# Kernel optimization log

Measured on AMD Instinct MI355X. Metric: run time of the kernel, lower is better.

The kernel has to match this reference:

```python
import jax, jax.numpy as jnp
import numpy as np

N = 50000
E = 800000
DIM_IN = 128
DIM_H = 16
HEADS = 8
DIM_OUT = 16
NEG_SLOPE = 0.2


def setup_inputs() -> dict:
    key = jax.random.key(0)
    ks = jax.random.split(key, 12)
    def glorot(k, shape):
        fan_in = shape[0]
        return jax.random.normal(k, shape, dtype=jnp.float32) / np.sqrt(fan_in)
    x = jax.random.normal(ks[0], (N, DIM_IN), dtype=jnp.float32)
    edge_index = jax.random.randint(ks[1], (2, E), 0, N, dtype=jnp.int64)
    # layer 1: GATv2Conv(dim_in, dim_h, heads=8)
    Wl1 = glorot(ks[2], (DIM_IN, HEADS * DIM_H))
    Wr1 = glorot(ks[3], (DIM_IN, HEADS * DIM_H))
    att1 = glorot(ks[4], (HEADS, DIM_H))
    bias1 = jnp.zeros((HEADS * DIM_H,), dtype=jnp.float32)
    # layer 2: GATv2Conv(dim_h*heads, dim_out, heads=1)
    Wl2 = glorot(ks[5], (HEADS * DIM_H, DIM_OUT))
    Wr2 = glorot(ks[6], (HEADS * DIM_H, DIM_OUT))
    att2 = glorot(ks[7], (1, DIM_OUT))
    bias2 = jnp.zeros((DIM_OUT,), dtype=jnp.float32)
    return {"x": x, "edge_index": edge_index, "Wl1": Wl1, "Wr1": Wr1,
            "att1": att1, "bias1": bias1, "Wl2": Wl2, "Wr2": Wr2,
            "att2": att2, "bias2": bias2}


def gatv2_layer(x, src, dst, Wl, Wr, att, bias, n_nodes, heads, ch):
    # x: [N, F_in]; src/dst: [Etot] (self-loops included)
    xl = (x @ Wl).reshape(n_nodes, heads, ch)  # source transform
    xr = (x @ Wr).reshape(n_nodes, heads, ch)  # target transform
    e = jax.nn.leaky_relu(xl[src] + xr[dst], NEG_SLOPE)      # [Etot, H, C]
    logits = jnp.einsum('ehc,hc->eh', e, att)                # [Etot, H]
    # segment softmax over incoming edges of each target node
    m = jax.ops.segment_max(logits, dst, num_segments=n_nodes)
    a = jnp.exp(logits - m[dst])
    denom = jax.ops.segment_sum(a, dst, num_segments=n_nodes)
    alpha = a / denom[dst]                                   # [Etot, H]
    out = jax.ops.segment_sum(xl[src] * alpha[:, :, None], dst,
                              num_segments=n_nodes)          # [N, H, C]
    return out.reshape(n_nodes, heads * ch) + bias


def reference(x, edge_index, Wl1, Wr1, att1, bias1, Wl2, Wr2, att2, bias2):
    # PyG GATv2Conv adds self-loops by default
    loops = jnp.arange(N, dtype=edge_index.dtype)
    src = jnp.concatenate([edge_index[0], loops])
    dst = jnp.concatenate([edge_index[1], loops])
    # dropout is identity in eval mode
    h = gatv2_layer(x, src, dst, Wl1, Wr1, att1, bias1, N, HEADS, DIM_H)
    h = jax.nn.elu(h)
    h = gatv2_layer(h, src, dst, Wl2, Wr2, att2, bias2, N, 1, DIM_OUT)
    return h, jax.nn.log_softmax(h, axis=1)
```

## Files before the change

kernel.cpp:

```cpp
#include <hip/hip_runtime.h>
#include <hip/hip_bf16.h>
#include <math.h>

#define NN 50000
#define EE 800000
#define DIN 128
#define HEADS 8
#define DH 16
#define DOUT 16
#define NEG 0.2f
#define GM 32
#define GB ((NN + GM - 1) / GM)
#define NB ((NN + 255) / 256)
#define DEGB ((EE / 4 + 255) / 256)
#define PAD 64

typedef __attribute__((ext_vector_type(8))) short bf16x8;
typedef __attribute__((ext_vector_type(4))) float f32x4;

__device__ __forceinline__ unsigned pack2bf(float a, float b) {
    union { __hip_bfloat162 h; unsigned u; } c;
    c.h = __float22bfloat162_rn(make_float2(a, b));
    return c.u;
}
__device__ __forceinline__ unsigned short f2bf(float v) {
    union { __hip_bfloat16 h; unsigned short u; } c;
    c.h = __float2bfloat16(v);
    return c.u;
}
__device__ __forceinline__ float bflo(unsigned u) { return __uint_as_float(u << 16); }
__device__ __forceinline__ float bfhi(unsigned u) { return __uint_as_float(u & 0xffff0000u); }

__global__ __launch_bounds__(256) void init_wcvt(int* __restrict__ cnt,
                                                 int* __restrict__ esrcPad,
                                                 const float* __restrict__ Wl,
                                                 const float* __restrict__ Wr,
                                                 unsigned short* __restrict__ Wb,
                                                 const float* __restrict__ Wl2,
                                                 const float* __restrict__ Wr2,
                                                 unsigned short* __restrict__ Wb2) {
    int b = blockIdx.x, t = threadIdx.x;
    if (b < NB) {
        int i = b * 256 + t;
        if (i < NN) {
            cnt[i] = 1;
            esrcPad[(size_t)i * PAD] = i;
        }
    } else if (b < NB + 128) {
        int i = (b - NB) * 256 + t;
        int n = i >> 7, k = i & 127;
        float v = (n < 128) ? Wl[k * 128 + n] : Wr[k * 128 + (n - 128)];
        Wb[i] = f2bf(v);
    } else {
        int i = (b - NB - 128) * 256 + t;
        int n = i >> 7, k = i & 127;
        float v = (n < 16) ? Wl2[k * 16 + n] : Wr2[k * 16 + (n - 16)];
        Wb2[i] = f2bf(v);
    }
}

__global__ __launch_bounds__(256) void fill_gemm1(const int* __restrict__ ei,
                                                  int* __restrict__ cnt,
                                                  int* __restrict__ esrcPad,
                                                  const float* __restrict__ x,
                                                  const unsigned short* __restrict__ Wb,
                                                  unsigned short* __restrict__ xlb,
                                                  float* __restrict__ xr) {
    __shared__ unsigned short As[GM][136];
    int t = threadIdx.x;
    if (blockIdx.x < DEGB) {
        int i = blockIdx.x * 256 + t;
        if (i >= EE / 4) return;
        int4 ss = ((const int4*)ei)[i];
        int4 dd = ((const int4*)(ei + EE))[i];
        int p;
        p = atomicAdd(&cnt[dd.x], 1); esrcPad[(size_t)dd.x * PAD + p] = ss.x;
        p = atomicAdd(&cnt[dd.y], 1); esrcPad[(size_t)dd.y * PAD + p] = ss.y;
        p = atomicAdd(&cnt[dd.z], 1); esrcPad[(size_t)dd.z * PAD + p] = ss.z;
        p = atomicAdd(&cnt[dd.w], 1); esrcPad[(size_t)dd.w * PAD + p] = ss.w;
        return;
    }
    int n0 = (blockIdx.x - DEGB) * GM;
    {
        int row = t >> 3, seg = t & 7;
        int nsrc = n0 + row < NN ? n0 + row : NN - 1;
        const float4* xp = (const float4*)(x + (size_t)nsrc * DIN + 16 * seg);
        float4 v0 = xp[0], v1 = xp[1], v2 = xp[2], v3 = xp[3];
        uint4 p0 = make_uint4(pack2bf(v0.x, v0.y), pack2bf(v0.z, v0.w),
                              pack2bf(v1.x, v1.y), pack2bf(v1.z, v1.w));
        uint4 p1 = make_uint4(pack2bf(v2.x, v2.y), pack2bf(v2.z, v2.w),
                              pack2bf(v3.x, v3.y), pack2bf(v3.z, v3.w));
        *(uint4*)&As[row][16 * seg]     = p0;
        *(uint4*)&As[row][16 * seg + 8] = p1;
    }
    __syncthreads();
    int lane = t & 63, w = t >> 6;
    int m = lane & 15, quad = lane >> 4;
    f32x4 acc[2][4];
#pragma unroll
    for (int mt = 0; mt < 2; ++mt)
#pragma unroll
        for (int nt = 0; nt < 4; ++nt) acc[mt][nt] = (f32x4){0.f, 0.f, 0.f, 0.f};
#pragma unroll
    for (int ks = 0; ks < 4; ++ks) {
        int k = 32 * ks + 8 * quad;
        bf16x8 a0 = *(const bf16x8*)&As[m][k];
        bf16x8 a1 = *(const bf16x8*)&As[16 + m][k];
#pragma unroll
        for (int nt = 0; nt < 4; ++nt) {
            int n = 64 * w + 16 * nt + m;
            bf16x8 b = *(const bf16x8*)(Wb + (size_t)n * 128 + k);
            acc[0][nt] = __builtin_amdgcn_mfma_f32_16x16x32_bf16(a0, b, acc[0][nt], 0, 0, 0);
            acc[1][nt] = __builtin_amdgcn_mfma_f32_16x16x32_bf16(a1, b, acc[1][nt], 0, 0, 0);
        }
    }
#pragma unroll
    for (int mt = 0; mt < 2; ++mt) {
#pragma unroll
        for (int nt = 0; nt < 4; ++nt) {
            int col = 64 * w + 16 * nt + m;
            int rbase = n0 + 16 * mt + 4 * quad;
            if (col < 128) {
#pragma unroll
                for (int r = 0; r < 4; ++r) {
                    int row = rbase + r;
                    if (row < NN) xlb[(size_t)row * DIN + col] = f2bf(acc[mt][nt][r]);
                }
            } else {
#pragma unroll
                for (int r = 0; r < 4; ++r) {
                    int row = rbase + r;
                    if (row < NN) xr[(size_t)row * DIN + (col - 128)] = acc[mt][nt][r];
                }
            }
        }
    }
}

__global__ __launch_bounds__(256) void l1_fused(const int* __restrict__ esrcPad,
                                                const int* __restrict__ cnt,
                                                const unsigned short* __restrict__ xlb,
                                                const float* __restrict__ xr,
                                                const float* __restrict__ att,
                                                const float* __restrict__ bias,
                                                unsigned short* __restrict__ hb) {
    int d = blockIdx.x * 4 + (threadIdx.x >> 6);
    int lane = threadIdx.x & 63;
    int quarter = lane >> 4;
    int q16 = lane & 15;
    int rs = d * PAD;
    int re = rs + cnt[d];
    int last = re - 1;
    float4 xr0 = ((const float4*)(xr + (size_t)d * DIN))[2 * q16];
    float4 xr1 = ((const float4*)(xr + (size_t)d * DIN))[2 * q16 + 1];
    float4 at0 = ((const float4*)att)[2 * q16];
    float4 at1 = ((const float4*)att)[2 * q16 + 1];
    float4 a0 = make_float4(0.f, 0.f, 0.f, 0.f);
    float4 a1 = make_float4(0.f, 0.f, 0.f, 0.f);
    float l = 0.f;
    int slot = rs + quarter;
    int c0 = slot < last ? slot : last;
    int s0 = esrcPad[c0];
    int c1 = slot + 4 < last ? slot + 4 : last;
    int s1 = esrcPad[c1];
    uint4 row = ((const uint4*)(xlb + (size_t)s0 * DIN))[q16];
    for (; slot < re; slot += 4) {
        uint4 cur = row;
        int c2 = slot + 8 < last ? slot + 8 : last;
        int s2 = esrcPad[c2];
        row = ((const uint4*)(xlb + (size_t)s1 * DIN))[q16];
        s1 = s2;
        float f0 = bflo(cur.x), f1 = bfhi(cur.x);
        float f2 = bflo(cur.y), f3 = bfhi(cur.y);
        float f4 = bflo(cur.z), f5 = bfhi(cur.z);
        float f6 = bflo(cur.w), f7 = bfhi(cur.w);
        float v0 = f0 + xr0.x; v0 = fmaxf(v0, NEG * v0);
        float v1 = f1 + xr0.y; v1 = fmaxf(v1, NEG * v1);
        float v2 = f2 + xr0.z; v2 = fmaxf(v2, NEG * v2);
        float v3 = f3 + xr0.w; v3 = fmaxf(v3, NEG * v3);
        float v4 = f4 + xr1.x; v4 = fmaxf(v4, NEG * v4);
        float v5 = f5 + xr1.y; v5 = fmaxf(v5, NEG * v5);
        float v6 = f6 + xr1.z; v6 = fmaxf(v6, NEG * v6);
        float v7 = f7 + xr1.w; v7 = fmaxf(v7, NEG * v7);
        float w = at0.x * v0 + at0.y * v1 + at0.z * v2 + at0.w * v3
                + at1.x * v4 + at1.y * v5 + at1.z * v6 + at1.w * v7;
        w += __shfl_xor(w, 1);
        float p = __expf(w);
        a0.x += p * f0; a0.y += p * f1; a0.z += p * f2; a0.w += p * f3;
        a1.x += p * f4; a1.y += p * f5; a1.z += p * f6; a1.w += p * f7;
        l += p;
    }
#pragma unroll
    for (int off = 16; off < 64; off <<= 1) {
        a0.x += __shfl_xor(a0.x, off); a0.y += __shfl_xor(a0.y, off);
        a0.z += __shfl_xor(a0.z, off); a0.w += __shfl_xor(a0.w, off);
        a1.x += __shfl_xor(a1.x, off); a1.y += __shfl_xor(a1.y, off);
        a1.z += __shfl_xor(a1.z, off); a1.w += __shfl_xor(a1.w, off);
        l += __shfl_xor(l, off);
    }
    if (quarter == 0) {
        float inv = 1.f / l;
        float4 b0 = ((const float4*)bias)[2 * q16];
        float4 b1 = ((const float4*)bias)[2 * q16 + 1];
        float4 o0, o1;
        o0.x = a0.x * inv + b0.x; o0.x = o0.x > 0.f ? o0.x : expm1f(o0.x);
        o0.y = a0.y * inv + b0.y; o0.y = o0.y > 0.f ? o0.y : expm1f(o0.y);
        o0.z = a0.z * inv + b0.z; o0.z = o0.z > 0.f ? o0.z : expm1f(o0.z);
        o0.w = a0.w * inv + b0.w; o0.w = o0.w > 0.f ? o0.w : expm1f(o0.w);
        o1.x = a1.x * inv + b1.x; o1.x = o1.x > 0.f ? o1.x : expm1f(o1.x);
        o1.y = a1.y * inv + b1.y; o1.y = o1.y > 0.f ? o1.y : expm1f(o1.y);
        o1.z = a1.z * inv + b1.z; o1.z = o1.z > 0.f ? o1.z : expm1f(o1.z);
        o1.w = a1.w * inv + b1.w; o1.w = o1.w > 0.f ? o1.w : expm1f(o1.w);
        uint4 pk = make_uint4(pack2bf(o0.x, o0.y), pack2bf(o0.z, o0.w),
                              pack2bf(o1.x, o1.y), pack2bf(o1.z, o1.w));
        ((uint4*)(hb + (size_t)d * DIN))[q16] = pk;
    }
}

__global__ __launch_bounds__(256) void gemm2(const unsigned short* __restrict__ hb,
                                             const unsigned short* __restrict__ Wb2,
                                             float* __restrict__ xl2, float* __restrict__ xr2) {
    __shared__ unsigned short As[GM][136];
    int t = threadIdx.x;
    int n0 = blockIdx.x * GM;
    {
        int row = t >> 3, s8 = t & 7;
        int nsrc = n0 + row < NN ? n0 + row : NN - 1;
        const uint4* src = (const uint4*)(hb + (size_t)nsrc * DIN);
        *(uint4*)&As[row][8 * s8]      = src[s8];
        *(uint4*)&As[row][8 * s8 + 64] = src[s8 + 8];
    }
    __syncthreads();
    int lane = t & 63, w = t >> 6;
    int m = lane & 15, quad = lane >> 4;
    int mt = w & 1, nt = w >> 1;
    f32x4 acc = (f32x4){0.f, 0.f, 0.f, 0.f};
#pragma unroll
    for (int ks = 0; ks < 4; ++ks) {
        int k = 32 * ks + 8 * quad;
        bf16x8 a = *(const bf16x8*)&As[16 * mt + m][k];
        bf16x8 b = *(const bf16x8*)(Wb2 + (size_t)(16 * nt + m) * 128 + k);
        acc = __builtin_amdgcn_mfma_f32_16x16x32_bf16(a, b, acc, 0, 0, 0);
    }
    float* __restrict__ dst = (nt == 0) ? xl2 : xr2;
#pragma unroll
    for (int r = 0; r < 4; ++r) {
        int node = n0 + 16 * mt + 4 * quad + r;
        if (node < NN) dst[(size_t)node * DOUT + m] = acc[r];
    }
}

__global__ __launch_bounds__(256) void l2_fused(const int* __restrict__ esrcPad,
                                                const int* __restrict__ cnt,
                                                const float* __restrict__ xl,
                                                const float* __restrict__ xr,
                                                const float* __restrict__ att,
                                                const float* __restrict__ bias,
                                                float* __restrict__ out) {
    int d = blockIdx.x * 4 + (threadIdx.x >> 6);
    int lane = threadIdx.x & 63;
    int sl = lane >> 2;
    int q = lane & 3;
    int rs = d * PAD;
    int re = rs + cnt[d];
    int last = re - 1;
    float4 xrq = ((const float4*)(xr + (size_t)d * DOUT))[q];
    float4 atq = ((const float4*)att)[q];
    float4 acc = make_float4(0.f, 0.f, 0.f, 0.f);
    float l = 0.f;
    int slot = rs + sl;
    int c0 = slot < last ? slot : last;
    int s0 = esrcPad[c0];
    for (; slot < re; slot += 16) {
        int c1 = slot + 16 < last ? slot + 16 : last;
        int s1 = esrcPad[c1];
        float4 cur = ((const float4*)(xl + (size_t)s0 * DOUT))[q];
        s0 = s1;
        float v0 = cur.x + xrq.x; v0 = fmaxf(v0, NEG * v0);
        float v1 = cur.y + xrq.y; v1 = fmaxf(v1, NEG * v1);
        float v2 = cur.z + xrq.z; v2 = fmaxf(v2, NEG * v2);
        float v3 = cur.w + xrq.w; v3 = fmaxf(v3, NEG * v3);
        float w = atq.x * v0 + atq.y * v1 + atq.z * v2 + atq.w * v3;
        w += __shfl_xor(w, 1);
        w += __shfl_xor(w, 2);
        float p = __expf(w);
        acc.x += p * cur.x; acc.y += p * cur.y;
        acc.z += p * cur.z; acc.w += p * cur.w;
        l += p;
    }
#pragma unroll
    for (int off = 4; off < 64; off <<= 1) {
        acc.x += __shfl_xor(acc.x, off);
        acc.y += __shfl_xor(acc.y, off);
        acc.z += __shfl_xor(acc.z, off);
        acc.w += __shfl_xor(acc.w, off);
        l += __shfl_xor(l, off);
    }
    float inv = 1.f / l;
    float4 b = ((const float4*)bias)[q];
    float4 v;
    v.x = acc.x * inv + b.x; v.y = acc.y * inv + b.y;
    v.z = acc.z * inv + b.z; v.w = acc.w * inv + b.w;
    float m = fmaxf(fmaxf(v.x, v.y), fmaxf(v.z, v.w));
    m = fmaxf(m, __shfl_xor(m, 1));
    m = fmaxf(m, __shfl_xor(m, 2));
    float es = __expf(v.x - m) + __expf(v.y - m) + __expf(v.z - m) + __expf(v.w - m);
    es += __shfl_xor(es, 1);
    es += __shfl_xor(es, 2);
    float lse = m + __logf(es);
    if (sl == 0) {
        ((float4*)(out + (size_t)d * DOUT))[q] = v;
        float4 ls;
        ls.x = v.x - lse; ls.y = v.y - lse; ls.z = v.z - lse; ls.w = v.w - lse;
        ((float4*)(out + (size_t)NN * DOUT + (size_t)d * DOUT))[q] = ls;
    }
}

extern "C" void kernel_launch(void* const* d_in, const int* in_sizes, int n_in,
                              void* d_out, int out_size, void* d_ws, size_t ws_size,
                              hipStream_t stream) {
    const float* x     = (const float*)d_in[0];
    const int*   ei    = (const int*)d_in[1];
    const float* Wl1   = (const float*)d_in[2];
    const float* Wr1   = (const float*)d_in[3];
    const float* att1  = (const float*)d_in[4];
    const float* bias1 = (const float*)d_in[5];
    const float* Wl2   = (const float*)d_in[6];
    const float* Wr2   = (const float*)d_in[7];
    const float* att2  = (const float*)d_in[8];
    const float* bias2 = (const float*)d_in[9];
    float* out = (float*)d_out;

    float* xr1    = (float*)d_ws;
    float* xl2    = xr1 + (size_t)NN * DIN;
    float* xr2    = xl2 + (size_t)NN * DOUT;
    unsigned short* xlb = (unsigned short*)(xr2 + (size_t)NN * DOUT);
    unsigned short* hb  = xlb + (size_t)NN * DIN;
    unsigned short* Wb  = hb + (size_t)NN * DIN;
    unsigned short* Wb2 = Wb + 256 * 128;
    int*   esrcPad = (int*)(Wb2 + 32 * 128);
    int*   cnt    = esrcPad + (size_t)NN * PAD;

    const int B = 256;
    init_wcvt<<<NB + 144, B, 0, stream>>>(cnt, esrcPad, Wl1, Wr1, Wb, Wl2, Wr2, Wb2);
    fill_gemm1<<<DEGB + GB, B, 0, stream>>>(ei, cnt, esrcPad, x, Wb, xlb, xr1);

    l1_fused<<<NN / 4, B, 0, stream>>>(esrcPad, cnt, xlb, xr1, att1, bias1, hb);

    gemm2<<<GB, B, 0, stream>>>(hb, Wb2, xl2, xr2);

    l2_fused<<<NN / 4, B, 0, stream>>>(esrcPad, cnt, xl2, xr2, att2, bias2, out);
}
```

Baseline: 236.7 us.

## Partition edge bucketing by destination range, shrink source indices to 16-bit

The CSR-fill phase now launches eight blocks per edge chunk. Each block handles only destinations in its own node-id range, so atomics and scattered writes from one block land in a narrower region of memory. The padded source-index array is stored as unsigned short instead of int, which halves its footprint and the bytes the aggregation kernels read. Nontemporal loads and stores are added for the edge list, the x input and the xr output. The price is reading the edge list eight times. The 16-bit indices are only valid because N is below 65536, and l1_fused/l2_fused must now read 16-bit indices correctly through the changed pointer type.

Measured after the change: 237.9 us. Within noise of the previous version (+0.5%).

```diff
diff --git a/kernel.cpp b/kernel.cpp
--- a/kernel.cpp
+++ b/kernel.cpp
@@ -13,10 +13,14 @@
 #define GB ((NN + GM - 1) / GM)
 #define NB ((NN + 255) / 256)
 #define DEGB ((EE / 4 + 255) / 256)
+#define NPART 8
+#define RANGE (NN / NPART)
+#define FILLB (DEGB * NPART)
 #define PAD 64
 
 typedef __attribute__((ext_vector_type(8))) short bf16x8;
 typedef __attribute__((ext_vector_type(4))) float f32x4;
+typedef __attribute__((ext_vector_type(4))) int i32x4;
 
 __device__ __forceinline__ unsigned pack2bf(float a, float b) {
     union { __hip_bfloat162 h; unsigned u; } c;
@@ -32,7 +36,7 @@
 __device__ __forceinline__ float bfhi(unsigned u) { return __uint_as_float(u & 0xffff0000u); }
 
 __global__ __launch_bounds__(256) void init_wcvt(int* __restrict__ cnt,
-                                                 int* __restrict__ esrcPad,
+                                                 unsigned short* __restrict__ esrcPad,
                                                  const float* __restrict__ Wl,
                                                  const float* __restrict__ Wr,
                                                  unsigned short* __restrict__ Wb,
@@ -44,7 +48,7 @@
         int i = b * 256 + t;
         if (i < NN) {
             cnt[i] = 1;
-            esrcPad[(size_t)i * PAD] = i;
+            esrcPad[(size_t)i * PAD] = (unsigned short)i;
         }
     } else if (b < NB + 128) {
         int i = (b - NB) * 256 + t;
@@ -61,35 +65,53 @@
 
 __global__ __launch_bounds__(256) void fill_gemm1(const int* __restrict__ ei,
                                                   int* __restrict__ cnt,
-                                                  int* __restrict__ esrcPad,
+                                                  unsigned short* __restrict__ esrcPad,
                                                   const float* __restrict__ x,
                                                   const unsigned short* __restrict__ Wb,
                                                   unsigned short* __restrict__ xlb,
                                                   float* __restrict__ xr) {
     __shared__ unsigned short As[GM][136];
     int t = threadIdx.x;
-    if (blockIdx.x < DEGB) {
-        int i = blockIdx.x * 256 + t;
+    if (blockIdx.x < FILLB) {
+        int chunk = blockIdx.x >> 3;
+        int r = blockIdx.x & 7;
+        int i = chunk * 256 + t;
         if (i >= EE / 4) return;
-        int4 ss = ((const int4*)ei)[i];
-        int4 dd = ((const int4*)(ei + EE))[i];
+        i32x4 ss = __builtin_nontemporal_load(((const i32x4*)ei) + i);
+        i32x4 dd = __builtin_nontemporal_load(((const i32x4*)(ei + EE)) + i);
+        int lo = r * RANGE;
         int p;
-        p = atomicAdd(&cnt[dd.x], 1); esrcPad[(size_t)dd.x * PAD + p] = ss.x;
-        p = atomicAdd(&cnt[dd.y], 1); esrcPad[(size_t)dd.y * PAD + p] = ss.y;
-        p = atomicAdd(&cnt[dd.z], 1); esrcPad[(size_t)dd.z * PAD + p] = ss.z;
-        p = atomicAdd(&cnt[dd.w], 1); esrcPad[(size_t)dd.w * PAD + p] = ss.w;
+        if ((unsigned)(dd[0] - lo) < RANGE) {
+            p = atomicAdd(&cnt[dd[0]], 1);
+            esrcPad[(size_t)dd[0] * PAD + p] = (unsigned short)ss[0];
+        }
+        if ((unsigned)(dd[1] - lo) < RANGE) {
+            p = atomicAdd(&cnt[dd[1]], 1);
+            esrcPad[(size_t)dd[1] * PAD + p] = (unsigned short)ss[1];
+        }
+        if ((unsigned)(dd[2] - lo) < RANGE) {
+            p = atomicAdd(&cnt[dd[2]], 1);
+            esrcPad[(size_t)dd[2] * PAD + p] = (unsigned short)ss[2];
+        }
+        if ((unsigned)(dd[3] - lo) < RANGE) {
+            p = atomicAdd(&cnt[dd[3]], 1);
+            esrcPad[(size_t)dd[3] * PAD + p] = (unsigned short)ss[3];
+        }
         return;
     }
-    int n0 = (blockIdx.x - DEGB) * GM;
+    int n0 = (blockIdx.x - FILLB) * GM;
     {
         int row = t >> 3, seg = t & 7;
         int nsrc = n0 + row < NN ? n0 + row : NN - 1;
-        const float4* xp = (const float4*)(x + (size_t)nsrc * DIN + 16 * seg);
-        float4 v0 = xp[0], v1 = xp[1], v2 = xp[2], v3 = xp[3];
-        uint4 p0 = make_uint4(pack2bf(v0.x, v0.y), pack2bf(v0.z, v0.w),
-                              pack2bf(v1.x, v1.y), pack2bf(v1.z, v1.w));
-        uint4 p1 = make_uint4(pack2bf(v2.x, v2.y), pack2bf(v2.z, v2.w),
-                              pack2bf(v3.x, v3.y), pack2bf(v3.z, v3.w));
+        const f32x4* xp = (const f32x4*)(x + (size_t)nsrc * DIN + 16 * seg);
+        f32x4 v0 = __builtin_nontemporal_load(xp);
+        f32x4 v1 = __builtin_nontemporal_load(xp + 1);
+        f32x4 v2 = __builtin_nontemporal_load(xp + 2);
+        f32x4 v3 = __builtin_nontemporal_load(xp + 3);
+        uint4 p0 = make_uint4(pack2bf(v0[0], v0[1]), pack2bf(v0[2], v0[3]),
+                              pack2bf(v1[0], v1[1]), pack2bf(v1[2], v1[3]));
+        uint4 p1 = make_uint4(pack2bf(v2[0], v2[1]), pack2bf(v2[2], v2[3]),
+                              pack2bf(v3[0], v3[1]), pack2bf(v3[2], v3[3]));
         *(uint4*)&As[row][16 * seg]     = p0;
         *(uint4*)&As[row][16 * seg + 8] = p1;
     }
@@ -130,14 +152,16 @@
 #pragma unroll
                 for (int r = 0; r < 4; ++r) {
                     int row = rbase + r;
-                    if (row < NN) xr[(size_t)row * DIN + (col - 128)] = acc[mt][nt][r];
+                    if (row < NN)
+                        __builtin_nontemporal_store(acc[mt][nt][r],
+                                                    &xr[(size_t)row * DIN + (col - 128)]);
                 }
             }
         }
     }
 }
 
-__global__ __launch_bounds__(256) void l1_fused(const int* __restrict__ esrcPad,
+__global__ __launch_bounds__(256) void l1_fused(const unsigned short* __restrict__ esrcPad,
                                                 const int* __restrict__ cnt,
                                                 const unsigned short* __restrict__ xlb,
                                                 const float* __restrict__ xr,
@@ -250,7 +274,7 @@
     }
 }
 
-__global__ __launch_bounds__(256) void l2_fused(const int* __restrict__ esrcPad,
+__global__ __launch_bounds__(256) void l2_fused(const unsigned short* __restrict__ esrcPad,
                                                 const int* __restrict__ cnt,
                                                 const float* __restrict__ xl,
                                                 const float* __restrict__ xr,
@@ -338,12 +362,12 @@
     unsigned short* hb  = xlb + (size_t)NN * DIN;
     unsigned short* Wb  = hb + (size_t)NN * DIN;
     unsigned short* Wb2 = Wb + 256 * 128;
-    int*   esrcPad = (int*)(Wb2 + 32 * 128);
-    int*   cnt    = esrcPad + (size_t)NN * PAD;
+    unsigned short* esrcPad = Wb2 + 32 * 128;
+    int*   cnt    = (int*)(esrcPad + (size_t)NN * PAD);
 
     const int B = 256;
     init_wcvt<<<NB + 144, B, 0, stream>>>(cnt, esrcPad, Wl1, Wr1, Wb, Wl2, Wr2, Wb2);
-    fill_gemm1<<<DEGB + GB, B, 0, stream>>>(ei, cnt, esrcPad, x, Wb, xlb, xr1);
+    fill_gemm1<<<FILLB + GB, B, 0, stream>>>(ei, cnt, esrcPad, x, Wb, xlb, xr1);
 
     l1_fused<<<NN / 4, B, 0, stream>>>(esrcPad, cnt, xlb, xr1, att1, bias1, hb);
 
```
